# Kernel tuning notes

Measured on AMD Instinct MI355X. Metric: run time of the kernel, lower is better.

The kernel has to match this reference:

```python
import jax, jax.numpy as jnp
import numpy as np

N, E, C, FIN, FOUT = 4096, 5, 2, 128, 64
DENSITY = 0.01


def setup_inputs() -> dict:
    key = jax.random.key(0)
    ks = jax.random.split(key, 8)
    vals = jax.random.uniform(ks[0], (E, N, N), dtype=jnp.float32)
    mask = jax.random.uniform(ks[1], (E, N, N)) < DENSITY
    A = jnp.where(mask, vals, 0.0)                      # [E,N,N] edge-type adjacencies (A[e,u,v]: u->v)
    h = jax.random.normal(ks[2], (N, FIN), dtype=jnp.float32)
    W1_0 = 0.01 * jax.random.normal(ks[3], (C, E), dtype=jnp.float32)  # GTConv init: normal(std=0.01)
    W2_0 = 0.01 * jax.random.normal(ks[4], (C, E), dtype=jnp.float32)
    W1_1 = 0.01 * jax.random.normal(ks[5], (C, E), dtype=jnp.float32)
    gcn_W = jax.random.normal(ks[6], (C, FIN, FOUT), dtype=jnp.float32) / np.sqrt(FIN)
    gcn_b = jnp.zeros((C, FOUT), dtype=jnp.float32)
    return {"A": A, "h": h, "W1_0": W1_0, "W2_0": W2_0, "W1_1": W1_1,
            "gcn_W": gcn_W, "gcn_b": gcn_b}


def reference(A, h, W1_0, W2_0, W1_1, gcn_W, gcn_b):
    # Structural support of the summed graphs (union of edge-type edges).
    mask = (A != 0).any(axis=0)                         # [N,N]

    def gtconv(filt):
        # weighted sum of edge-type adjacencies per channel: dgl.adj_sum_graph
        return jnp.einsum('ce,euv->cuv', filt, A)       # [C,N,N]

    def right_norm(M, sum_axis):
        # EdgeWeightNorm(norm='right'): divide each edge weight by total in-weight at dst
        d = M.sum(axis=sum_axis, keepdims=True)
        return M / jnp.where(d != 0, d, 1.0)

    def softmax_norm(S):
        # exp on existing edges only, then right-normalize over in-edges (src axis=1)
        w = jnp.where(mask, jnp.exp(S), 0.0)
        return right_norm(w, sum_axis=1)

    # Layer 0 (first=True)
    RA = softmax_norm(gtconv(W1_0))                     # first_adj, [C,N,N]
    RB = softmax_norm(gtconv(W2_0))
    H0 = jnp.einsum('cuk,ckv->cuv', RA, RB)             # dgl.adj_product_graph
    # Layer 1 (first=False): result_A = H0, result_B = conv1(A) (no softmax)
    RB1 = gtconv(W1_1)
    H1 = jnp.einsum('cuk,ckv->cuv', H0, RB1)

    layers = jnp.stack([RA, H0, H1], axis=1)            # [C,3,N,N] = layer_list per channel
    Wn = right_norm(layers, sum_axis=2)                 # right norm over src (axis u)
    # GraphConv(norm='none', activation=relu) with edge_weight: out[v] = relu(sum_u w[u,v] h[u] W + b)
    agg = jnp.einsum('cluv,uf->clvf', Wn, h)            # [C,3,N,FIN]
    out = jax.nn.relu(jnp.einsum('clvf,cfo->clvo', agg, gcn_W) + gcn_b[:, None, None, :])
    return out                                          # [C,3,N,FOUT]
```

## Files before the change

kernel.cpp:

```cpp
#include <hip/hip_runtime.h>

#define NN    4096
#define NE    5
#define NC    2
#define FINF  128
#define FOUTF 64
#define CAP   384


union f16u { unsigned short s; _Float16 h; };

static __device__ __forceinline__ unsigned short f2h(float x)
{
    f16u u; u.h = (_Float16)x; return u.s;
}
static __device__ __forceinline__ float lo16f(unsigned x)
{
    f16u u; u.s = (unsigned short)(x & 0xffff); return (float)u.h;
}
static __device__ __forceinline__ float hi16f(unsigned x)
{
    f16u u; u.s = (unsigned short)(x >> 16); return (float)u.h;
}
static __device__ __forceinline__ unsigned pack2h(float a, float b)
{
    return (unsigned)f2h(a) | ((unsigned)f2h(b) << 16);
}

__global__ __launch_bounds__(256) void init_misc(int4* __restrict__ cnt4,
                                                 const float4* __restrict__ h4,
                                                 uint2* __restrict__ hh)
{
    int b = blockIdx.x;
    if (b < 4) {
        cnt4[b * 256 + threadIdx.x] = int4{0, 0, 0, 0};
    } else {
        int i = (b - 4) * 256 + threadIdx.x;
        float4 f = h4[i];
        uint2 r;
        r.x = pack2h(f.x, f.y);
        r.y = pack2h(f.z, f.w);
        hh[i] = r;
    }
}

__global__ __launch_bounds__(256) void build_csc(
    const float* __restrict__ A,
    const float* __restrict__ W1_0,
    const float* __restrict__ W2_0,
    const float* __restrict__ W1_1,
    int*  __restrict__ cnt,
    int4* __restrict__ epack)
{
    float fA0[NE], fA1[NE], fB0[NE], fB1[NE], fC0[NE], fC1[NE];
#pragma unroll
    for (int e = 0; e < NE; ++e) {
        fA0[e] = W1_0[e];      fA1[e] = W1_0[NE + e];
        fB0[e] = W2_0[e];      fB1[e] = W2_0[NE + e];
        fC0[e] = W1_1[e];      fC1[e] = W1_1[NE + e];
    }

    const size_t S = (size_t)NN * NN / 4;
    const float4* A4 = (const float4*)A;
    size_t stride = (size_t)gridDim.x * blockDim.x;
    for (size_t i = (size_t)blockIdx.x * blockDim.x + threadIdx.x; i < S; i += stride) {
        float4 q0 = A4[i];
        float4 q1 = A4[i + S];
        float4 q2 = A4[i + 2 * S];
        float4 q3 = A4[i + 3 * S];
        float4 q4 = A4[i + 4 * S];
        int u  = (int)(i >> 10);
        int v0 = ((int)i & 1023) << 2;
#define DO_COMP(comp, joff)                                                      \
        {                                                                        \
            float a0 = q0.comp, a1 = q1.comp, a2 = q2.comp,                      \
                  a3 = q3.comp, a4 = q4.comp;                                    \
            if (a0 != 0.f || a1 != 0.f || a2 != 0.f || a3 != 0.f || a4 != 0.f) { \
                float sA0 = fA0[0]*a0 + fA0[1]*a1 + fA0[2]*a2 + fA0[3]*a3 + fA0[4]*a4; \
                float sA1 = fA1[0]*a0 + fA1[1]*a1 + fA1[2]*a2 + fA1[3]*a3 + fA1[4]*a4; \
                float sB0 = fB0[0]*a0 + fB0[1]*a1 + fB0[2]*a2 + fB0[3]*a3 + fB0[4]*a4; \
                float sB1 = fB1[0]*a0 + fB1[1]*a1 + fB1[2]*a2 + fB1[3]*a3 + fB1[4]*a4; \
                float sC0 = fC0[0]*a0 + fC0[1]*a1 + fC0[2]*a2 + fC0[3]*a3 + fC0[4]*a4; \
                float sC1 = fC1[0]*a0 + fC1[1]*a1 + fC1[2]*a2 + fC1[3]*a3 + fC1[4]*a4; \
                int v = v0 + joff;                                               \
                int pos = atomicAdd(&cnt[v], 1);                                 \
                if (pos < CAP) {                                                 \
                    int4 rec;                                                    \
                    rec.x = u;                                                   \
                    rec.y = (int)pack2h(__expf(sA0), __expf(sA1));               \
                    rec.z = (int)pack2h(__expf(sB0), __expf(sB1));               \
                    rec.w = (int)pack2h(sC0, sC1);                               \
                    epack[v * CAP + pos] = rec;                                  \
                }                                                                \
            }                                                                    \
        }
        DO_COMP(x, 0)
        DO_COMP(y, 1)
        DO_COMP(z, 2)
        DO_COMP(w, 3)
#undef DO_COMP
    }
}

template<int STAGE>
__global__ __launch_bounds__(256) void spmm_col(
    const int*   __restrict__ cnt,
    const int4*  __restrict__ epack,
    const uint2* __restrict__ Xh_in,
    const float* __restrict__ Dd_in,
    const float* __restrict__ gW,
    const float* __restrict__ gb,
    float*       __restrict__ out,
    unsigned short* __restrict__ Xh_out,
    float*       __restrict__ Dd_out)
{
    int v = blockIdx.x;
    int n = cnt[v];
    if (n > CAP) n = CAP;

    __shared__ float4 s_e[CAP];
    __shared__ float  s_red[4];
    __shared__ float4 s_acc[NC][8][32];
    __shared__ float  s_y[NC][FINF];
    __shared__ float  s_inv[NC];

    int tid = threadIdx.x;
    if (tid < 4) s_red[tid] = 0.f;
    __syncthreads();

    float l0 = 0.f, l1 = 0.f, ld0 = 0.f, ld1 = 0.f;
    for (int i = tid; i < n; i += 256) {
        int4 E = epack[v * CAP + i];
        unsigned wb = (unsigned)((STAGE == 0) ? E.y : (STAGE == 1) ? E.z : E.w);
        float w0 = lo16f(wb), w1 = hi16f(wb);
        s_e[i] = float4{__int_as_float(E.x), w0, w1, 0.f};
        l0 += w0;
        l1 += w1;
        if (STAGE != 0) {
            ld0 += w0 * Dd_in[E.x];
            ld1 += w1 * Dd_in[NN + E.x];
        }
    }
    if (STAGE == 0) { ld0 = l0; ld1 = l1; }

#pragma unroll
    for (int m = 32; m >= 1; m >>= 1) {
        l0  += __shfl_xor(l0,  m);
        l1  += __shfl_xor(l1,  m);
        ld0 += __shfl_xor(ld0, m);
        ld1 += __shfl_xor(ld1, m);
    }
    if ((tid & 63) == 0) {
        atomicAdd(&s_red[0], l0);
        atomicAdd(&s_red[1], l1);
        atomicAdd(&s_red[2], ld0);
        atomicAdd(&s_red[3], ld1);
    }
    __syncthreads();

    int grp = tid >> 5, lane = tid & 31;
    float4 a0 = {0.f, 0.f, 0.f, 0.f};
    float4 a1 = {0.f, 0.f, 0.f, 0.f};

    if (STAGE == 0) {
#pragma unroll 2
        for (int i = grp; i < n; i += 8) {
            float4 e = s_e[i];
            uint2 b = Xh_in[(size_t)__float_as_int(e.x) * 32 + lane];
            float x0 = lo16f(b.x), x1 = hi16f(b.x);
            float x2 = lo16f(b.y), x3 = hi16f(b.y);
            a0.x += e.y * x0; a0.y += e.y * x1; a0.z += e.y * x2; a0.w += e.y * x3;
            a1.x += e.z * x0; a1.y += e.z * x1; a1.z += e.z * x2; a1.w += e.z * x3;
        }
    } else {
        const uint2* P0 = Xh_in;
        const uint2* P1 = Xh_in + (size_t)NN * 32;
#pragma unroll 2
        for (int i = grp; i < n; i += 8) {
            float4 e = s_e[i];
            int u = __float_as_int(e.x);
            uint2 b0 = P0[(size_t)u * 32 + lane];
            uint2 b1 = P1[(size_t)u * 32 + lane];
            a0.x += e.y * lo16f(b0.x); a0.y += e.y * hi16f(b0.x);
            a0.z += e.y * lo16f(b0.y); a0.w += e.y * hi16f(b0.y);
            a1.x += e.z * lo16f(b1.x); a1.y += e.z * hi16f(b1.x);
            a1.z += e.z * lo16f(b1.y); a1.w += e.z * hi16f(b1.y);
        }
    }

    s_acc[0][grp][lane] = a0;
    s_acc[1][grp][lane] = a1;
    __syncthreads();

    int c = tid >> 7, f = tid & 127;
    {
        const float* base = (const float*)s_acc[c];
        float s = 0.f;
#pragma unroll
        for (int g = 0; g < 8; ++g) s += base[g * 128 + f];

        float inv = 1.f;
        if (STAGE < 2 && n > 0) inv = 1.f / s_red[c];
        float val = s * inv;

        s_y[c][f] = val;
        if (STAGE < 2)
            Xh_out[((size_t)c * NN + v) * FINF + f] = f2h(val);
        if (f == 0) {
            float dvn = s_red[2 + c] * inv;
            s_inv[c] = (dvn != 0.f) ? (1.f / dvn) : 1.f;
            if (STAGE < 2) Dd_out[c * NN + v] = dvn;
        }
    }
    __syncthreads();

    if (tid < 2 * FOUTF) {
        int c2 = tid >> 6, o = tid & 63;
        const float* w = gW + (size_t)c2 * FINF * FOUTF + o;
        const float* y = s_y[c2];
        float acc = 0.f;
#pragma unroll 8
        for (int f2 = 0; f2 < FINF; ++f2)
            acc += y[f2] * w[(size_t)f2 * FOUTF];
        float r = acc * s_inv[c2] + gb[c2 * FOUTF + o];
        out[(((size_t)c2 * 3 + STAGE) * NN + v) * FOUTF + o] = fmaxf(r, 0.f);
    }
}

extern "C" void kernel_launch(void* const* d_in, const int* in_sizes, int n_in,
                              void* d_out, int out_size, void* d_ws, size_t ws_size,
                              hipStream_t stream)
{
    const float* A     = (const float*)d_in[0];
    const float* h     = (const float*)d_in[1];
    const float* W1_0  = (const float*)d_in[2];
    const float* W2_0  = (const float*)d_in[3];
    const float* W1_1  = (const float*)d_in[4];
    const float* gW    = (const float*)d_in[5];
    const float* gb    = (const float*)d_in[6];
    float* out = (float*)d_out;

    char* ws = (char*)d_ws;
    int*            cnt   = (int*)(ws);
    int4*           epack = (int4*)(ws + 16384);
    float*          DdA   = (float*)(ws + 25182208);
    float*          Dd1   = (float*)(ws + 25214976);
    uint2*          hh    = (uint2*)(ws + 25247744);
    unsigned short* XhA   = (unsigned short*)(ws + 26296320);
    unsigned short* Xh1   = (unsigned short*)(ws + 28393472);

    init_misc<<<516, 256, 0, stream>>>((int4*)cnt, (const float4*)h, hh);
    build_csc<<<2048, 256, 0, stream>>>(A, W1_0, W2_0, W1_1, cnt, epack);

    spmm_col<0><<<NN, 256, 0, stream>>>(cnt, epack, hh, nullptr, gW, gb, out, XhA, DdA);
    spmm_col<1><<<NN, 256, 0, stream>>>(cnt, epack, (const uint2*)XhA, DdA, gW, gb, out, Xh1, Dd1);
    spmm_col<2><<<NN, 256, 0, stream>>>(cnt, epack, (const uint2*)Xh1, Dd1, gW, gb, out, nullptr, nullptr);
}
```

Baseline: 212.1 us.

## Use nontemporal A loads, 16-byte gathers in SpMM, split GCN matvec across all threads

The CSC build now streams the dense adjacency with nontemporal loads, which hint to the cache that the data will not be reused. The SpMM gather switches from 8-byte to 16-byte loads: 16-lane groups handle 8 features each, so 16 edges are processed per pass instead of 8, with the shared-memory reduction reindexed to match. The final 128x64 GCN matvec now uses all 256 threads by splitting the input dimension in half and combining the halves with a lane shuffle. Risks are higher register use per thread and fewer load instructions in flight per edge.

```diff
diff --git a/kernel.cpp b/kernel.cpp
--- a/kernel.cpp
+++ b/kernel.cpp
@@ -6,6 +6,8 @@
 #define FINF  128
 #define FOUTF 64
 #define CAP   384
+
+typedef float vf4 __attribute__((ext_vector_type(4)));
 
 
 union f16u { unsigned short s; _Float16 h; };
@@ -61,20 +63,19 @@
     }
 
     const size_t S = (size_t)NN * NN / 4;
-    const float4* A4 = (const float4*)A;
+    const vf4* A4 = (const vf4*)A;
     size_t stride = (size_t)gridDim.x * blockDim.x;
     for (size_t i = (size_t)blockIdx.x * blockDim.x + threadIdx.x; i < S; i += stride) {
-        float4 q0 = A4[i];
-        float4 q1 = A4[i + S];
-        float4 q2 = A4[i + 2 * S];
-        float4 q3 = A4[i + 3 * S];
-        float4 q4 = A4[i + 4 * S];
+        vf4 q0 = __builtin_nontemporal_load(A4 + i);
+        vf4 q1 = __builtin_nontemporal_load(A4 + i + S);
+        vf4 q2 = __builtin_nontemporal_load(A4 + i + 2 * S);
+        vf4 q3 = __builtin_nontemporal_load(A4 + i + 3 * S);
+        vf4 q4 = __builtin_nontemporal_load(A4 + i + 4 * S);
         int u  = (int)(i >> 10);
         int v0 = ((int)i & 1023) << 2;
-#define DO_COMP(comp, joff)                                                      \
+#define DO_COMP(j)                                                               \
         {                                                                        \
-            float a0 = q0.comp, a1 = q1.comp, a2 = q2.comp,                      \
-                  a3 = q3.comp, a4 = q4.comp;                                    \
+            float a0 = q0[j], a1 = q1[j], a2 = q2[j], a3 = q3[j], a4 = q4[j];    \
             if (a0 != 0.f || a1 != 0.f || a2 != 0.f || a3 != 0.f || a4 != 0.f) { \
                 float sA0 = fA0[0]*a0 + fA0[1]*a1 + fA0[2]*a2 + fA0[3]*a3 + fA0[4]*a4; \
                 float sA1 = fA1[0]*a0 + fA1[1]*a1 + fA1[2]*a2 + fA1[3]*a3 + fA1[4]*a4; \
@@ -82,7 +83,7 @@
                 float sB1 = fB1[0]*a0 + fB1[1]*a1 + fB1[2]*a2 + fB1[3]*a3 + fB1[4]*a4; \
                 float sC0 = fC0[0]*a0 + fC0[1]*a1 + fC0[2]*a2 + fC0[3]*a3 + fC0[4]*a4; \
                 float sC1 = fC1[0]*a0 + fC1[1]*a1 + fC1[2]*a2 + fC1[3]*a3 + fC1[4]*a4; \
-                int v = v0 + joff;                                               \
+                int v = v0 + j;                                                  \
                 int pos = atomicAdd(&cnt[v], 1);                                 \
                 if (pos < CAP) {                                                 \
                     int4 rec;                                                    \
@@ -94,10 +95,10 @@
                 }                                                                \
             }                                                                    \
         }
-        DO_COMP(x, 0)
-        DO_COMP(y, 1)
-        DO_COMP(z, 2)
-        DO_COMP(w, 3)
+        DO_COMP(0)
+        DO_COMP(1)
+        DO_COMP(2)
+        DO_COMP(3)
 #undef DO_COMP
     }
 }
@@ -106,7 +107,7 @@
 __global__ __launch_bounds__(256) void spmm_col(
     const int*   __restrict__ cnt,
     const int4*  __restrict__ epack,
-    const uint2* __restrict__ Xh_in,
+    const unsigned short* __restrict__ Xh_in,
     const float* __restrict__ Dd_in,
     const float* __restrict__ gW,
     const float* __restrict__ gb,
@@ -120,7 +121,7 @@
 
     __shared__ float4 s_e[CAP];
     __shared__ float  s_red[4];
-    __shared__ float4 s_acc[NC][8][32];
+    __shared__ float4 s_acc4[NC][2][16][16];
     __shared__ float  s_y[NC][FINF];
     __shared__ float  s_inv[NC];
 
@@ -158,46 +159,58 @@
     }
     __syncthreads();
 
-    int grp = tid >> 5, lane = tid & 31;
-    float4 a0 = {0.f, 0.f, 0.f, 0.f};
-    float4 a1 = {0.f, 0.f, 0.f, 0.f};
+    int grp = tid >> 4, ln = tid & 15;
+    float a0[8], a1[8];
+#pragma unroll
+    for (int k = 0; k < 8; ++k) { a0[k] = 0.f; a1[k] = 0.f; }
 
     if (STAGE == 0) {
-#pragma unroll 2
-        for (int i = grp; i < n; i += 8) {
+        const uint4* H = (const uint4*)Xh_in;
+        for (int i = grp; i < n; i += 16) {
             float4 e = s_e[i];
-            uint2 b = Xh_in[(size_t)__float_as_int(e.x) * 32 + lane];
+            uint4 b = H[(size_t)__float_as_int(e.x) * 16 + ln];
             float x0 = lo16f(b.x), x1 = hi16f(b.x);
             float x2 = lo16f(b.y), x3 = hi16f(b.y);
-            a0.x += e.y * x0; a0.y += e.y * x1; a0.z += e.y * x2; a0.w += e.y * x3;
-            a1.x += e.z * x0; a1.y += e.z * x1; a1.z += e.z * x2; a1.w += e.z * x3;
+            float x4 = lo16f(b.z), x5 = hi16f(b.z);
+            float x6 = lo16f(b.w), x7 = hi16f(b.w);
+            a0[0] += e.y * x0; a0[1] += e.y * x1; a0[2] += e.y * x2; a0[3] += e.y * x3;
+            a0[4] += e.y * x4; a0[5] += e.y * x5; a0[6] += e.y * x6; a0[7] += e.y * x7;
+            a1[0] += e.z * x0; a1[1] += e.z * x1; a1[2] += e.z * x2; a1[3] += e.z * x3;
+            a1[4] += e.z * x4; a1[5] += e.z * x5; a1[6] += e.z * x6; a1[7] += e.z * x7;
         }
     } else {
-        const uint2* P0 = Xh_in;
-        const uint2* P1 = Xh_in + (size_t)NN * 32;
-#pragma unroll 2
-        for (int i = grp; i < n; i += 8) {
+        const uint4* P0 = (const uint4*)Xh_in;
+        const uint4* P1 = P0 + (size_t)NN * 16;
+        for (int i = grp; i < n; i += 16) {
             float4 e = s_e[i];
             int u = __float_as_int(e.x);
-            uint2 b0 = P0[(size_t)u * 32 + lane];
-            uint2 b1 = P1[(size_t)u * 32 + lane];
-            a0.x += e.y * lo16f(b0.x); a0.y += e.y * hi16f(b0.x);
-            a0.z += e.y * lo16f(b0.y); a0.w += e.y * hi16f(b0.y);
-            a1.x += e.z * lo16f(b1.x); a1.y += e.z * hi16f(b1.x);
-            a1.z += e.z * lo16f(b1.y); a1.w += e.z * hi16f(b1.y);
-        }
-    }
-
-    s_acc[0][grp][lane] = a0;
-    s_acc[1][grp][lane] = a1;
+            uint4 b0 = P0[(size_t)u * 16 + ln];
+            uint4 b1 = P1[(size_t)u * 16 + ln];
+            a0[0] += e.y * lo16f(b0.x); a0[1] += e.y * hi16f(b0.x);
+            a0[2] += e.y * lo16f(b0.y); a0[3] += e.y * hi16f(b0.y);
+            a0[4] += e.y * lo16f(b0.z); a0[5] += e.y * hi16f(b0.z);
+            a0[6] += e.y * lo16f(b0.w); a0[7] += e.y * hi16f(b0.w);
+            a1[0] += e.z * lo16f(b1.x); a1[1] += e.z * hi16f(b1.x);
+            a1[2] += e.z * lo16f(b1.y); a1[3] += e.z * hi16f(b1.y);
+            a1[4] += e.z * lo16f(b1.z); a1[5] += e.z * hi16f(b1.z);
+            a1[6] += e.z * lo16f(b1.w); a1[7] += e.z * hi16f(b1.w);
+        }
+    }
+
+    s_acc4[0][0][grp][ln] = float4{a0[0], a0[1], a0[2], a0[3]};
+    s_acc4[0][1][grp][ln] = float4{a0[4], a0[5], a0[6], a0[7]};
+    s_acc4[1][0][grp][ln] = float4{a1[0], a1[1], a1[2], a1[3]};
+    s_acc4[1][1][grp][ln] = float4{a1[4], a1[5], a1[6], a1[7]};
     __syncthreads();
 
     int c = tid >> 7, f = tid & 127;
     {
-        const float* base = (const float*)s_acc[c];
+        const float* sa = (const float*)s_acc4;
+        int k4 = (f >> 2) & 1, lnr = f >> 3, j = f & 3;
+        int base = c * 2048 + k4 * 1024 + lnr * 4 + j;
         float s = 0.f;
 #pragma unroll
-        for (int g = 0; g < 8; ++g) s += base[g * 128 + f];
+        for (int g = 0; g < 16; ++g) s += sa[base + g * 64];
 
         float inv = 1.f;
         if (STAGE < 2 && n > 0) inv = 1.f / s_red[c];
@@ -214,16 +227,19 @@
     }
     __syncthreads();
 
-    if (tid < 2 * FOUTF) {
-        int c2 = tid >> 6, o = tid & 63;
-        const float* w = gW + (size_t)c2 * FINF * FOUTF + o;
-        const float* y = s_y[c2];
+    {
+        int c2 = tid >> 7, o = (tid >> 1) & 63, half = tid & 1;
+        const float* y  = s_y[c2] + half * 64;
+        const float* wh = gW + (size_t)c2 * FINF * FOUTF + (size_t)half * 64 * FOUTF + o;
         float acc = 0.f;
 #pragma unroll 8
-        for (int f2 = 0; f2 < FINF; ++f2)
-            acc += y[f2] * w[(size_t)f2 * FOUTF];
-        float r = acc * s_inv[c2] + gb[c2 * FOUTF + o];
-        out[(((size_t)c2 * 3 + STAGE) * NN + v) * FOUTF + o] = fmaxf(r, 0.f);
+        for (int f2 = 0; f2 < 64; ++f2)
+            acc += y[f2] * wh[(size_t)f2 * FOUTF];
+        acc += __shfl_xor(acc, 1);
+        if (half == 0) {
+            float r = acc * s_inv[c2] + gb[c2 * FOUTF + o];
+            out[(((size_t)c2 * 3 + STAGE) * NN + v) * FOUTF + o] = fmaxf(r, 0.f);
+        }
     }
 }
 
@@ -252,7 +268,7 @@
     init_misc<<<516, 256, 0, stream>>>((int4*)cnt, (const float4*)h, hh);
     build_csc<<<2048, 256, 0, stream>>>(A, W1_0, W2_0, W1_1, cnt, epack);
 
-    spmm_col<0><<<NN, 256, 0, stream>>>(cnt, epack, hh, nullptr, gW, gb, out, XhA, DdA);
-    spmm_col<1><<<NN, 256, 0, stream>>>(cnt, epack, (const uint2*)XhA, DdA, gW, gb, out, Xh1, Dd1);
-    spmm_col<2><<<NN, 256, 0, stream>>>(cnt, epack, (const uint2*)Xh1, Dd1, gW, gb, out, nullptr, nullptr);
-}
+    spmm_col<0><<<NN, 256, 0, stream>>>(cnt, epack, (const unsigned short*)hh, nullptr, gW, gb, out, XhA, DdA);
+    spmm_col<1><<<NN, 256, 0, stream>>>(cnt, epack, XhA, DdA, gW, gb, out, Xh1, Dd1);
+    spmm_col<2><<<NN, 256, 0, stream>>>(cnt, epack, Xh1, Dd1, gW, gb, out, nullptr, nullptr);
+}
```

Measured after the change: 248.4 us. 17.1% more time.

## Split SpMM column blocks per channel and parallelize GCN projection across all threads

Applied to the files above, without the earlier changes.

Each spmm_col block now handles one (channel, column) pair, doubling the grid to NN*NC blocks, so each block does half the gather work and uses less shared memory. The final 128x64 projection is split over four 32-row partitions using all 256 threads, followed by a shared-memory reduction. In stage 0 the two channels no longer share a single gathered row of h, so that row is loaded twice, and the edge list is re-read once per channel. In exchange the kernel gets more parallelism and occupancy.

```diff
diff --git a/kernel.cpp b/kernel.cpp
--- a/kernel.cpp
+++ b/kernel.cpp
@@ -106,7 +106,7 @@
 __global__ __launch_bounds__(256) void spmm_col(
     const int*   __restrict__ cnt,
     const int4*  __restrict__ epack,
-    const uint2* __restrict__ Xh_in,
+    const unsigned short* __restrict__ Xh_in,
     const float* __restrict__ Dd_in,
     const float* __restrict__ gW,
     const float* __restrict__ gb,
@@ -114,116 +114,102 @@
     unsigned short* __restrict__ Xh_out,
     float*       __restrict__ Dd_out)
 {
-    int v = blockIdx.x;
+    int c = blockIdx.x & 1;
+    int v = blockIdx.x >> 1;
     int n = cnt[v];
     if (n > CAP) n = CAP;
 
-    __shared__ float4 s_e[CAP];
-    __shared__ float  s_red[4];
-    __shared__ float4 s_acc[NC][8][32];
-    __shared__ float  s_y[NC][FINF];
-    __shared__ float  s_inv[NC];
+    __shared__ float2 s_e[CAP];
+    __shared__ float  s_red[2];
+    __shared__ float4 s_acc[8][32];
+    __shared__ float  s_y[FINF];
+    __shared__ float  s_part[4][FOUTF];
+    __shared__ float  s_inv;
 
     int tid = threadIdx.x;
-    if (tid < 4) s_red[tid] = 0.f;
-    __syncthreads();
-
-    float l0 = 0.f, l1 = 0.f, ld0 = 0.f, ld1 = 0.f;
+    if (tid < 2) s_red[tid] = 0.f;
+    __syncthreads();
+
+    float l = 0.f, ld = 0.f;
     for (int i = tid; i < n; i += 256) {
         int4 E = epack[v * CAP + i];
         unsigned wb = (unsigned)((STAGE == 0) ? E.y : (STAGE == 1) ? E.z : E.w);
-        float w0 = lo16f(wb), w1 = hi16f(wb);
-        s_e[i] = float4{__int_as_float(E.x), w0, w1, 0.f};
-        l0 += w0;
-        l1 += w1;
-        if (STAGE != 0) {
-            ld0 += w0 * Dd_in[E.x];
-            ld1 += w1 * Dd_in[NN + E.x];
-        }
-    }
-    if (STAGE == 0) { ld0 = l0; ld1 = l1; }
+        float w = c ? hi16f(wb) : lo16f(wb);
+        s_e[i] = float2{__int_as_float(E.x), w};
+        l += w;
+        if (STAGE != 0) ld += w * Dd_in[c * NN + E.x];
+    }
+    if (STAGE == 0) ld = l;
 
 #pragma unroll
     for (int m = 32; m >= 1; m >>= 1) {
-        l0  += __shfl_xor(l0,  m);
-        l1  += __shfl_xor(l1,  m);
-        ld0 += __shfl_xor(ld0, m);
-        ld1 += __shfl_xor(ld1, m);
+        l  += __shfl_xor(l,  m);
+        ld += __shfl_xor(ld, m);
     }
     if ((tid & 63) == 0) {
-        atomicAdd(&s_red[0], l0);
-        atomicAdd(&s_red[1], l1);
-        atomicAdd(&s_red[2], ld0);
-        atomicAdd(&s_red[3], ld1);
+        atomicAdd(&s_red[0], l);
+        atomicAdd(&s_red[1], ld);
     }
     __syncthreads();
 
     int grp = tid >> 5, lane = tid & 31;
-    float4 a0 = {0.f, 0.f, 0.f, 0.f};
-    float4 a1 = {0.f, 0.f, 0.f, 0.f};
-
-    if (STAGE == 0) {
+    float4 a = {0.f, 0.f, 0.f, 0.f};
+
+    {
+        const uint2* P = (const uint2*)Xh_in;
+        if (STAGE != 0) P += (size_t)c * NN * 32;
 #pragma unroll 2
         for (int i = grp; i < n; i += 8) {
-            float4 e = s_e[i];
-            uint2 b = Xh_in[(size_t)__float_as_int(e.x) * 32 + lane];
-            float x0 = lo16f(b.x), x1 = hi16f(b.x);
-            float x2 = lo16f(b.y), x3 = hi16f(b.y);
-            a0.x += e.y * x0; a0.y += e.y * x1; a0.z += e.y * x2; a0.w += e.y * x3;
-            a1.x += e.z * x0; a1.y += e.z * x1; a1.z += e.z * x2; a1.w += e.z * x3;
+            float2 e = s_e[i];
+            uint2 b = P[(size_t)__float_as_int(e.x) * 32 + lane];
+            a.x += e.y * lo16f(b.x);
+            a.y += e.y * hi16f(b.x);
+            a.z += e.y * lo16f(b.y);
+            a.w += e.y * hi16f(b.y);
         }
-    } else {
-        const uint2* P0 = Xh_in;
-        const uint2* P1 = Xh_in + (size_t)NN * 32;
-#pragma unroll 2
-        for (int i = grp; i < n; i += 8) {
-            float4 e = s_e[i];
-            int u = __float_as_int(e.x);
-            uint2 b0 = P0[(size_t)u * 32 + lane];
-            uint2 b1 = P1[(size_t)u * 32 + lane];
-            a0.x += e.y * lo16f(b0.x); a0.y += e.y * hi16f(b0.x);
-            a0.z += e.y * lo16f(b0.y); a0.w += e.y * hi16f(b0.y);
-            a1.x += e.z * lo16f(b1.x); a1.y += e.z * hi16f(b1.x);
-            a1.z += e.z * lo16f(b1.y); a1.w += e.z * hi16f(b1.y);
-        }
-    }
-
-    s_acc[0][grp][lane] = a0;
-    s_acc[1][grp][lane] = a1;
-    __syncthreads();
-
-    int c = tid >> 7, f = tid & 127;
-    {
-        const float* base = (const float*)s_acc[c];
+    }
+
+    s_acc[grp][lane] = a;
+    __syncthreads();
+
+    if (tid < FINF) {
+        int f = tid;
+        const float* base = (const float*)s_acc;
         float s = 0.f;
 #pragma unroll
         for (int g = 0; g < 8; ++g) s += base[g * 128 + f];
 
         float inv = 1.f;
-        if (STAGE < 2 && n > 0) inv = 1.f / s_red[c];
+        if (STAGE < 2 && n > 0) inv = 1.f / s_red[0];
         float val = s * inv;
 
-        s_y[c][f] = val;
+        s_y[f] = val;
         if (STAGE < 2)
             Xh_out[((size_t)c * NN + v) * FINF + f] = f2h(val);
         if (f == 0) {
-            float dvn = s_red[2 + c] * inv;
-            s_inv[c] = (dvn != 0.f) ? (1.f / dvn) : 1.f;
+            float dvn = s_red[1] * inv;
+            s_inv = (dvn != 0.f) ? (1.f / dvn) : 1.f;
             if (STAGE < 2) Dd_out[c * NN + v] = dvn;
         }
     }
     __syncthreads();
 
-    if (tid < 2 * FOUTF) {
-        int c2 = tid >> 6, o = tid & 63;
-        const float* w = gW + (size_t)c2 * FINF * FOUTF + o;
-        const float* y = s_y[c2];
+    {
+        int p = tid >> 6, o = tid & 63;
+        const float* y = s_y + p * 32;
+        const float* w = gW + (size_t)c * FINF * FOUTF + (size_t)p * 32 * FOUTF + o;
         float acc = 0.f;
 #pragma unroll 8
-        for (int f2 = 0; f2 < FINF; ++f2)
+        for (int f2 = 0; f2 < 32; ++f2)
             acc += y[f2] * w[(size_t)f2 * FOUTF];
-        float r = acc * s_inv[c2] + gb[c2 * FOUTF + o];
-        out[(((size_t)c2 * 3 + STAGE) * NN + v) * FOUTF + o] = fmaxf(r, 0.f);
+        s_part[p][o] = acc;
+    }
+    __syncthreads();
+    if (tid < FOUTF) {
+        int o = tid;
+        float acc = s_part[0][o] + s_part[1][o] + s_part[2][o] + s_part[3][o];
+        float r = acc * s_inv + gb[c * FOUTF + o];
+        out[(((size_t)c * 3 + STAGE) * NN + v) * FOUTF + o] = fmaxf(r, 0.f);
     }
 }
 
@@ -252,7 +238,7 @@
     init_misc<<<516, 256, 0, stream>>>((int4*)cnt, (const float4*)h, hh);
     build_csc<<<2048, 256, 0, stream>>>(A, W1_0, W2_0, W1_1, cnt, epack);
 
-    spmm_col<0><<<NN, 256, 0, stream>>>(cnt, epack, hh, nullptr, gW, gb, out, XhA, DdA);
-    spmm_col<1><<<NN, 256, 0, stream>>>(cnt, epack, (const uint2*)XhA, DdA, gW, gb, out, Xh1, Dd1);
-    spmm_col<2><<<NN, 256, 0, stream>>>(cnt, epack, (const uint2*)Xh1, Dd1, gW, gb, out, nullptr, nullptr);
-}
+    spmm_col<0><<<NN * NC, 256, 0, stream>>>(cnt, epack, (const unsigned short*)hh, nullptr, gW, gb, out, XhA, DdA);
+    spmm_col<1><<<NN * NC, 256, 0, stream>>>(cnt, epack, XhA, DdA, gW, gb, out, Xh1, Dd1);
+    spmm_col<2><<<NN * NC, 256, 0, stream>>>(cnt, epack, Xh1, Dd1, gW, gb, out, nullptr, nullptr);
+}
```

Result: slower. 226.0 us (+6.5%).
